# Kernel optimization log

Measured on AMD Instinct MI355X. Metric: run time of the kernel, lower is better.

## Reference

```python
import jax, jax.numpy as jnp
import numpy as np

B, N = 32, 512
NODE_F, EDGE_F = 64, 16
OUT = [64, 64, 64, 128]
TARGET = 16
DEGS = [1, 2, 3, 4]  # degree buckets (degree 0 filtered out, as in init_duvenaud)


def setup_inputs() -> dict:
    key = jax.random.key(0)
    ks = jax.random.split(key, 12)
    # adjacency: each node v connects to v+1..v+deg(v) (mod N), deg in {1..4}
    deg = jax.random.randint(ks[0], (B, N), 1, 5)
    off = jnp.arange(1, 5)                                   # (4,)
    cols = (jnp.arange(N)[:, None] + off[None, :]) % N       # (N,4)
    vals = (off[None, None, :] <= deg[:, :, None]).astype(jnp.float32)  # (B,N,4)
    g = jnp.zeros((B, N, N), jnp.float32).at[:, jnp.arange(N)[:, None], cols].set(vals)
    h_in = jax.random.normal(ks[1], (B, N, NODE_F), jnp.float32)
    e = jax.random.normal(ks[2], (B, N, N, EDGE_F), jnp.float32)
    # per-timestep, per-degree update matrices H_t: (n_deg, msg_in_t, out_t)
    ins = [NODE_F + EDGE_F, OUT[0] + EDGE_F, OUT[1] + EDGE_F]
    H0 = jax.random.normal(ks[3], (len(DEGS), ins[0], OUT[0]), jnp.float32)
    H1 = jax.random.normal(ks[4], (len(DEGS), ins[1], OUT[1]), jnp.float32)
    H2 = jax.random.normal(ks[5], (len(DEGS), ins[2], OUT[2]), jnp.float32)
    # readout matrices W_l for each of the 4 stored layers h^0..h^3
    layer_in = [NODE_F, OUT[0], OUT[1], OUT[2]]
    W0 = jax.random.normal(ks[6], (layer_in[0], OUT[3]), jnp.float32)
    W1 = jax.random.normal(ks[7], (layer_in[1], OUT[3]), jnp.float32)
    W2 = jax.random.normal(ks[8], (layer_in[2], OUT[3]), jnp.float32)
    W3 = jax.random.normal(ks[9], (layer_in[3], OUT[3]), jnp.float32)
    W_final = jax.random.normal(ks[10], (OUT[3], TARGET), jnp.float32) * 0.05
    b_final = jnp.zeros((TARGET,), jnp.float32)
    return {"g": g, "h_in": h_in, "e": e,
            "H0": H0, "H1": H1, "H2": H2,
            "W0": W0, "W1": W1, "W2": W2, "W3": W3,
            "W_final": W_final, "b_final": b_final}


def _step(g, e, h, H):
    # duvenaud message m_v = sum_w g[v,w] * cat(h_w, e_vw); split concat to avoid
    # materializing the (B,N,N,F+E) tensor the torch loop builds per node.
    mh = jnp.einsum('bvw,bwf->bvf', g, h)
    me = jnp.einsum('bvw,bvwe->bve', g, e)
    m = jnp.concatenate([mh, me], axis=-1)                 # (B,N,msg_in)
    deg = jnp.sum(g, axis=2)                               # (B,N) node degrees
    # degree-bucketed linear update: h'_v = m_v @ H[bucket(deg_v)]
    cand = jnp.einsum('bvm,dmo->bvdo', m, H)               # (B,N,n_deg,out)
    degs = jnp.asarray(DEGS, m.dtype)
    sel = (deg[:, :, None] == degs[None, None, :]).astype(m.dtype)  # one-hot bucket
    return jnp.einsum('bvd,bvdo->bvo', sel, cand)          # deg not in DEGS -> 0


def reference(g, h_in, e, H0, H1, H2, W0, W1, W2, W3, W_final, b_final):
    hs = [h_in]
    for H in (H0, H1, H2):
        hs.append(_step(g, e, hs[-1], H))
    # duvenaud readout: sum over layers/nodes of masked softmax(h_l @ W_l)
    acc = jnp.zeros((g.shape[0], W_final.shape[0]), h_in.dtype)
    for h, W in zip(hs, (W0, W1, W2, W3)):
        lin = jnp.einsum('bvf,fo->bvo', h, W)
        # mask rows whose linear output is all zero (padding / never-updated nodes)
        mask = (jnp.sum(lin != 0, axis=-1, keepdims=True) > 0).astype(lin.dtype)
        acc = acc + jnp.sum(jax.nn.softmax(lin, axis=-1) * mask, axis=1)
    out = acc @ W_final + b_final
    return jax.nn.softmax(out, axis=-1)
```

## Files before the change

### kernel.cpp

```cpp
#include <hip/hip_runtime.h>

#define BATCH 32
#define NN 512
#define NODE_F 64
#define EDGE_F 16
#define MSG 80
#define OUTF 64
#define RD 128
#define TGT 16
#define KMAX 8
#define ROWS (BATCH*NN)

__global__ __launch_bounds__(256) void preprocess_kernel(
    const float* __restrict__ g, const float* __restrict__ e,
    int* __restrict__ adj_idx, float* __restrict__ adj_val,
    int* __restrict__ nnzArr, int* __restrict__ bucketArr,
    float* __restrict__ me,
    float* __restrict__ h1, float* __restrict__ h2, float* __restrict__ h3,
    float* __restrict__ accv, int* __restrict__ counts)
{
  __shared__ int   s_idx[4][KMAX];
  __shared__ float s_val[4][KMAX];
  int tid  = threadIdx.x;
  int gtid = blockIdx.x * 256 + tid;
  if (gtid < BATCH*RD) accv[gtid] = 0.f;
  if (gtid < 4) counts[gtid] = 0;
  int lane = tid & 63;
  int wid  = tid >> 6;
  int row  = blockIdx.x * 4 + wid;
  const float* grow = g + (size_t)row * NN;
  float deg = 0.f;
  int cnt = 0;
  for (int it = 0; it < NN/64; ++it) {
    int w = it*64 + lane;
    float gv = grow[w];
    deg += gv;
    unsigned long long m = __ballot(gv != 0.0f);
    int before = __popcll(m & ((1ull << lane) - 1ull));
    if (gv != 0.0f) {
      int pos = cnt + before;
      if (pos < KMAX) { s_idx[wid][pos] = w; s_val[wid][pos] = gv; }
    }
    cnt += __popcll(m);
  }
  for (int off = 32; off; off >>= 1) deg += __shfl_xor(deg, off);
  __syncthreads();
  const float* erow = e + (size_t)row * NN * EDGE_F;
  if (cnt <= KMAX) {
    int k = lane >> 4, f = lane & 15;
    float part = 0.f;
    if (k < cnt)     part  = s_val[wid][k]   * erow[s_idx[wid][k]  *EDGE_F + f];
    if (cnt > 4) {
      int k2 = k + 4;
      if (k2 < cnt)  part += s_val[wid][k2]  * erow[s_idx[wid][k2] *EDGE_F + f];
    }
    part += __shfl_xor(part, 32);
    part += __shfl_xor(part, 16);
    if (lane < EDGE_F) me[(size_t)row*EDGE_F + lane] = part;
  } else {
    float mef = 0.f;
    for (int w = 0; w < NN; ++w) {
      float gv = grow[w];
      if (gv != 0.f && lane < EDGE_F) mef += gv * erow[w*EDGE_F + lane];
    }
    if (lane < EDGE_F) me[(size_t)row*EDGE_F + lane] = mef;
  }
  if (lane < KMAX && lane < cnt) {
    adj_idx[row*KMAX + lane] = s_idx[wid][lane];
    adj_val[row*KMAX + lane] = s_val[wid][lane];
  }
  int bk = -1;
  if      (deg == 1.0f) bk = 0;
  else if (deg == 2.0f) bk = 1;
  else if (deg == 3.0f) bk = 2;
  else if (deg == 4.0f) bk = 3;
  if (bk < 0) {
    h1[(size_t)row*NODE_F + lane] = 0.f;
    h2[(size_t)row*NODE_F + lane] = 0.f;
    h3[(size_t)row*NODE_F + lane] = 0.f;
  }
  if (lane == 0) {
    bucketArr[row] = bk;
    nnzArr[row] = cnt;
  }
}

__global__ __launch_bounds__(256) void scatter_kernel(
    const int* __restrict__ bucketArr,
    int* __restrict__ counts, int* __restrict__ perm)
{
  int i = blockIdx.x * blockDim.x + threadIdx.x;
  int lane = threadIdx.x & 63;
  int bk = bucketArr[i];
  #pragma unroll
  for (int d = 0; d < 4; ++d) {
    unsigned long long m = __ballot(bk == d);
    if (m == 0ull) continue;
    int leader = __ffsll((long long)m) - 1;
    int tot    = __popcll(m);
    int base = 0;
    if (lane == leader) base = atomicAdd(&counts[d], tot);
    base = __shfl(base, leader);
    if (bk == d) {
      int before = __popcll(m & ((1ull << lane) - 1ull));
      perm[d*ROWS + base + before] = i;
    }
  }
}

__global__ __launch_bounds__(256) void step_kernel(
    const float* __restrict__ h_prev, float* __restrict__ h_out,
    const float* __restrict__ Ht,
    const int* __restrict__ perm, const int* __restrict__ counts,
    const int* __restrict__ nnzArr, const int* __restrict__ adj_idx,
    const float* __restrict__ adj_val, const float* __restrict__ me,
    const float* __restrict__ g)
{
  int d = blockIdx.x >> 8;
  int chunk = blockIdx.x & 255;
  int cnt = counts[d];
  int base = chunk * 64;
  if (base >= cnt) return;
  __shared__ float smt[MSG][68];
  __shared__ float sH[MSG*OUTF];
  __shared__ int   srow[64];
  int tid = threadIdx.x;
  int lane = tid & 63, wid = tid >> 6;
  {
    const float4* H4 = (const float4*)(Ht + (size_t)d*MSG*OUTF);
    float4* s4 = (float4*)sH;
    for (int f = tid; f < MSG*OUTF/4; f += 256) s4[f] = H4[f];
  }
  #pragma unroll 2
  for (int t = 0; t < 16; ++t) {
    int nl = wid*16 + t;
    int gi = base + nl;
    float mh = 0.f;
    int row = -1;
    if (gi < cnt) {
      row = perm[d*ROWS + gi];
      int bb = row >> 9;
      int nnz = nnzArr[row];
      if (nnz <= KMAX) {
        int4   ai = *(const int4*)  &adj_idx[row*KMAX];
        float4 av = *(const float4*)&adj_val[row*KMAX];
        const float* hb = h_prev + (size_t)bb*NN*NODE_F + lane;
        if (nnz > 0) mh += av.x * hb[(size_t)ai.x*NODE_F];
        if (nnz > 1) mh += av.y * hb[(size_t)ai.y*NODE_F];
        if (nnz > 2) mh += av.z * hb[(size_t)ai.z*NODE_F];
        if (nnz > 3) mh += av.w * hb[(size_t)ai.w*NODE_F];
        if (nnz > 4) {
          int4   ai2 = *(const int4*)  &adj_idx[row*KMAX + 4];
          float4 av2 = *(const float4*)&adj_val[row*KMAX + 4];
          mh += av2.x * hb[(size_t)ai2.x*NODE_F];
          if (nnz > 5) mh += av2.y * hb[(size_t)ai2.y*NODE_F];
          if (nnz > 6) mh += av2.z * hb[(size_t)ai2.z*NODE_F];
          if (nnz > 7) mh += av2.w * hb[(size_t)ai2.w*NODE_F];
        }
      } else {
        const float* grow = g + (size_t)row * NN;
        for (int w = 0; w < NN; ++w) {
          float gv = grow[w];
          if (gv != 0.f) mh += gv * h_prev[((size_t)(bb*NN + w))*NODE_F + lane];
        }
      }
    }
    smt[lane][nl] = mh;
    if (lane < EDGE_F) smt[NODE_F + lane][nl] = (row >= 0) ? me[(size_t)row*EDGE_F + lane] : 0.f;
    if (lane == 0) srow[nl] = row;
  }
  __syncthreads();
  int tn = tid & 15, to = tid >> 4;
  float4 acc[4];
  acc[0] = acc[1] = acc[2] = acc[3] = make_float4(0.f,0.f,0.f,0.f);
  #pragma unroll 8
  for (int i = 0; i < MSG; ++i) {
    float4 hv = *(const float4*)&smt[i][4*tn];
    float4 wv = *(const float4*)&sH[i*OUTF + 4*to];
    float hk[4] = {hv.x, hv.y, hv.z, hv.w};
    #pragma unroll
    for (int k = 0; k < 4; ++k) {
      acc[k].x += hk[k]*wv.x; acc[k].y += hk[k]*wv.y;
      acc[k].z += hk[k]*wv.z; acc[k].w += hk[k]*wv.w;
    }
  }
  #pragma unroll
  for (int k = 0; k < 4; ++k) {
    int r = srow[4*tn + k];
    if (r >= 0) *(float4*)&h_out[(size_t)r*OUTF + 4*to] = acc[k];
  }
}

__global__ __launch_bounds__(256) void readout_kernel(
    const float* __restrict__ h0, const float* __restrict__ h1,
    const float* __restrict__ h2, const float* __restrict__ h3,
    const float* __restrict__ W0, const float* __restrict__ W1,
    const float* __restrict__ W2, const float* __restrict__ W3,
    float* __restrict__ accv)
{
  int l = blockIdx.x >> 8;
  int chunk = blockIdx.x & 255;
  const float* hs = (l==0)?h0:(l==1)?h1:(l==2)?h2:h3;
  const float* Wl = (l==0)?W0:(l==1)?W1:(l==2)?W2:W3;
  __shared__ float sW[NODE_F*RD];
  __shared__ float sht[NODE_F*68];
  __shared__ float snmax[64], snsum[64];
  __shared__ int   snflag[64];
  float* redm = sht;
  int*   redf = (int*)(sht + 64*17);
  int tid = threadIdx.x;
  {
    const float4* W4 = (const float4*)Wl;
    float4* sW4 = (float4*)sW;
    #pragma unroll
    for (int r = 0; r < 8; ++r) sW4[tid + 256*r] = W4[tid + 256*r];
    const float4* hv4 = (const float4*)(hs + (size_t)chunk*64*NODE_F);
    #pragma unroll
    for (int r = 0; r < 4; ++r) {
      int f = tid + 256*r;
      int n = f >> 4, c = f & 15;
      float4 v = hv4[f];
      sht[(4*c+0)*68 + n] = v.x;
      sht[(4*c+1)*68 + n] = v.y;
      sht[(4*c+2)*68 + n] = v.z;
      sht[(4*c+3)*68 + n] = v.w;
    }
  }
  __syncthreads();
  int tn = tid & 15, to = tid >> 4;
  int b = chunk >> 3;
  float4 accA[4], accB[4];
  #pragma unroll
  for (int k = 0; k < 4; ++k) { accA[k] = make_float4(0,0,0,0); accB[k] = make_float4(0,0,0,0); }
  #pragma unroll 4
  for (int i = 0; i < NODE_F; ++i) {
    float4 hv = *(const float4*)&sht[i*68 + 4*tn];
    float4 w0 = *(const float4*)&sW[i*128 + 8*to];
    float4 w1 = *(const float4*)&sW[i*128 + 8*to + 4];
    float hk[4] = {hv.x, hv.y, hv.z, hv.w};
    #pragma unroll
    for (int k = 0; k < 4; ++k) {
      accA[k].x += hk[k]*w0.x; accA[k].y += hk[k]*w0.y;
      accA[k].z += hk[k]*w0.z; accA[k].w += hk[k]*w0.w;
      accB[k].x += hk[k]*w1.x; accB[k].y += hk[k]*w1.y;
      accB[k].z += hk[k]*w1.z; accB[k].w += hk[k]*w1.w;
    }
  }
  __syncthreads();
  #pragma unroll
  for (int k = 0; k < 4; ++k) {
    float4 a = accA[k], bq = accB[k];
    float pm = fmaxf(fmaxf(fmaxf(a.x,a.y),fmaxf(a.z,a.w)),
                     fmaxf(fmaxf(bq.x,bq.y),fmaxf(bq.z,bq.w)));
    int nz = (a.x!=0.f)||(a.y!=0.f)||(a.z!=0.f)||(a.w!=0.f)||
             (bq.x!=0.f)||(bq.y!=0.f)||(bq.z!=0.f)||(bq.w!=0.f);
    int n = 4*tn + k;
    redm[n*17 + to] = pm;
    redf[n*17 + to] = nz;
  }
  __syncthreads();
  {
    int n = tid >> 2, sub = tid & 3;
    float m = redm[n*17 + sub*4 + 0];
    m = fmaxf(m, redm[n*17 + sub*4 + 1]);
    m = fmaxf(m, redm[n*17 + sub*4 + 2]);
    m = fmaxf(m, redm[n*17 + sub*4 + 3]);
    int f = redf[n*17 + sub*4 + 0] | redf[n*17 + sub*4 + 1] |
            redf[n*17 + sub*4 + 2] | redf[n*17 + sub*4 + 3];
    m = fmaxf(m, __shfl_xor(m, 1)); m = fmaxf(m, __shfl_xor(m, 2));
    f |= __shfl_xor(f, 1); f |= __shfl_xor(f, 2);
    if (sub == 0) { snmax[n] = m; snflag[n] = f; }
  }
  __syncthreads();
  #pragma unroll
  for (int k = 0; k < 4; ++k) {
    int n = 4*tn + k;
    float m = snmax[n];
    accA[k].x = __expf(accA[k].x - m); accA[k].y = __expf(accA[k].y - m);
    accA[k].z = __expf(accA[k].z - m); accA[k].w = __expf(accA[k].w - m);
    accB[k].x = __expf(accB[k].x - m); accB[k].y = __expf(accB[k].y - m);
    accB[k].z = __expf(accB[k].z - m); accB[k].w = __expf(accB[k].w - m);
    float ps = accA[k].x+accA[k].y+accA[k].z+accA[k].w+
               accB[k].x+accB[k].y+accB[k].z+accB[k].w;
    redm[n*17 + to] = ps;
  }
  __syncthreads();
  {
    int n = tid >> 2, sub = tid & 3;
    float s = redm[n*17 + sub*4 + 0] + redm[n*17 + sub*4 + 1] +
              redm[n*17 + sub*4 + 2] + redm[n*17 + sub*4 + 3];
    s += __shfl_xor(s, 1); s += __shfl_xor(s, 2);
    if (sub == 0) snsum[n] = s;
  }
  __syncthreads();
  float4 aj0 = make_float4(0,0,0,0), aj1 = make_float4(0,0,0,0);
  #pragma unroll
  for (int k = 0; k < 4; ++k) {
    int n = 4*tn + k;
    if (snflag[n]) {
      float inv = 1.0f / snsum[n];
      aj0.x += accA[k].x*inv; aj0.y += accA[k].y*inv;
      aj0.z += accA[k].z*inv; aj0.w += accA[k].w*inv;
      aj1.x += accB[k].x*inv; aj1.y += accB[k].y*inv;
      aj1.z += accB[k].z*inv; aj1.w += accB[k].w*inv;
    }
  }
  #pragma unroll
  for (int off = 1; off < 16; off <<= 1) {
    aj0.x += __shfl_xor(aj0.x, off); aj0.y += __shfl_xor(aj0.y, off);
    aj0.z += __shfl_xor(aj0.z, off); aj0.w += __shfl_xor(aj0.w, off);
    aj1.x += __shfl_xor(aj1.x, off); aj1.y += __shfl_xor(aj1.y, off);
    aj1.z += __shfl_xor(aj1.z, off); aj1.w += __shfl_xor(aj1.w, off);
  }
  if (tn == 0) {
    float* dst = &accv[b*RD + 8*to];
    atomicAdd(dst+0, aj0.x); atomicAdd(dst+1, aj0.y);
    atomicAdd(dst+2, aj0.z); atomicAdd(dst+3, aj0.w);
    atomicAdd(dst+4, aj1.x); atomicAdd(dst+5, aj1.y);
    atomicAdd(dst+6, aj1.z); atomicAdd(dst+7, aj1.w);
  }
}

__global__ __launch_bounds__(256) void final_kernel(
    const float* __restrict__ accv, const float* __restrict__ Wf,
    const float* __restrict__ bf, float* __restrict__ out)
{
  int b = blockIdx.x;
  int tid = threadIdx.x;
  int tg = tid & 15, part = tid >> 4;
  float p = 0.f;
  #pragma unroll
  for (int q = 0; q < 8; ++q) {
    int i = part*8 + q;
    p += accv[b*RD + i] * Wf[i*TGT + tg];
  }
  __shared__ float pp[16][17];
  pp[part][tg] = p;
  __syncthreads();
  if (tid < 16) {
    float v = bf[tid];
    #pragma unroll
    for (int q = 0; q < 16; ++q) v += pp[q][tid];
    float mx = v;
    for (int off = 8; off; off >>= 1) mx = fmaxf(mx, __shfl_xor(mx, off, 16));
    float e = __expf(v - mx);
    float s = e;
    for (int off = 8; off; off >>= 1) s += __shfl_xor(s, off, 16);
    out[b*TGT + tid] = e / s;
  }
}

extern "C" void kernel_launch(void* const* d_in, const int* in_sizes, int n_in,
                              void* d_out, int out_size, void* d_ws, size_t ws_size,
                              hipStream_t stream)
{
  const float* g    = (const float*)d_in[0];
  const float* h_in = (const float*)d_in[1];
  const float* e    = (const float*)d_in[2];
  const float* H0   = (const float*)d_in[3];
  const float* H1   = (const float*)d_in[4];
  const float* H2   = (const float*)d_in[5];
  const float* W0   = (const float*)d_in[6];
  const float* W1   = (const float*)d_in[7];
  const float* W2   = (const float*)d_in[8];
  const float* W3   = (const float*)d_in[9];
  const float* Wf   = (const float*)d_in[10];
  const float* bf   = (const float*)d_in[11];
  float* out = (float*)d_out;

  char* base = (char*)d_ws;
  size_t off = 0;
  auto alloc = [&](size_t bytes) -> void* {
    void* p = base + off;
    off = (off + bytes + 255) & ~(size_t)255;
    return p;
  };
  int*   adj_idx   = (int*)  alloc((size_t)ROWS*KMAX*sizeof(int));
  float* adj_val   = (float*)alloc((size_t)ROWS*KMAX*sizeof(float));
  int*   nnzArr    = (int*)  alloc((size_t)ROWS*sizeof(int));
  int*   bucketArr = (int*)  alloc((size_t)ROWS*sizeof(int));
  float* me        = (float*)alloc((size_t)ROWS*EDGE_F*sizeof(float));
  int*   perm      = (int*)  alloc((size_t)4*ROWS*sizeof(int));
  int*   counts    = (int*)  alloc(4*sizeof(int) + (size_t)BATCH*RD*sizeof(float));
  float* accv      = (float*)(counts + 4);
  float* h1        = (float*)alloc((size_t)ROWS*NODE_F*sizeof(float)*3);
  float* h2 = h1 + (size_t)ROWS*NODE_F;
  float* h3 = h2 + (size_t)ROWS*NODE_F;

  preprocess_kernel<<<ROWS/4, 256, 0, stream>>>(g, e, adj_idx, adj_val, nnzArr, bucketArr, me,
                                                h1, h2, h3, accv, counts);
  scatter_kernel<<<ROWS/256, 256, 0, stream>>>(bucketArr, counts, perm);
  step_kernel<<<4*256, 256, 0, stream>>>(h_in, h1, H0, perm, counts, nnzArr, adj_idx, adj_val, me, g);
  step_kernel<<<4*256, 256, 0, stream>>>(h1,   h2, H1, perm, counts, nnzArr, adj_idx, adj_val, me, g);
  step_kernel<<<4*256, 256, 0, stream>>>(h2,   h3, H2, perm, counts, nnzArr, adj_idx, adj_val, me, g);
  readout_kernel<<<4*256, 256, 0, stream>>>(h_in, h1, h2, h3, W0, W1, W2, W3, accv);
  final_kernel<<<BATCH, 256, 0, stream>>>(accv, Wf, bf, out);
}
```

Measured before the change: 770.5 us.

## Fuse layer-0 readout into scatter and final softmax into readout via last-block

Moves the layer-0 readout (which only needs h_in) into the scatter kernel as extra blocks, so it overlaps with the bucket scatter instead of running in the later readout. Merges the final projection and softmax into the readout kernel: the last block to finish, found with an atomic counter, does the final GEMV and softmax. This removes one kernel launch and shortens the tail of the readout, at the cost of a threadfence and atomic per block plus a serial single-block final stage.

```diff
diff --git a/kernel.cpp b/kernel.cpp
--- a/kernel.cpp
+++ b/kernel.cpp
@@ -10,6 +10,7 @@
 #define TGT 16
 #define KMAX 8
 #define ROWS (BATCH*NN)
+#define RB_TOTAL 768
 
 __global__ __launch_bounds__(256) void preprocess_kernel(
     const float* __restrict__ g, const float* __restrict__ e,
@@ -24,7 +25,7 @@
   int tid  = threadIdx.x;
   int gtid = blockIdx.x * 256 + tid;
   if (gtid < BATCH*RD) accv[gtid] = 0.f;
-  if (gtid < 4) counts[gtid] = 0;
+  if (gtid < 8) counts[gtid] = 0;
   int lane = tid & 63;
   int wid  = tid >> 6;
   int row  = blockIdx.x * 4 + wid;
@@ -85,26 +86,156 @@
   }
 }
 
-__global__ __launch_bounds__(256) void scatter_kernel(
+__device__ __forceinline__ void readout_block(
+    const float* __restrict__ hs, const float* __restrict__ Wl,
+    int chunk, float* __restrict__ accv,
+    float* sW, float* sht, float* snmax, float* snsum, int* snflag)
+{
+  float* redm = sht;
+  int*   redf = (int*)(sht + 64*17);
+  int tid = threadIdx.x;
+  {
+    const float4* W4 = (const float4*)Wl;
+    float4* sW4 = (float4*)sW;
+    #pragma unroll
+    for (int r = 0; r < 8; ++r) sW4[tid + 256*r] = W4[tid + 256*r];
+    const float4* hv4 = (const float4*)(hs + (size_t)chunk*64*NODE_F);
+    #pragma unroll
+    for (int r = 0; r < 4; ++r) {
+      int f = tid + 256*r;
+      int n = f >> 4, c = f & 15;
+      float4 v = hv4[f];
+      sht[(4*c+0)*68 + n] = v.x;
+      sht[(4*c+1)*68 + n] = v.y;
+      sht[(4*c+2)*68 + n] = v.z;
+      sht[(4*c+3)*68 + n] = v.w;
+    }
+  }
+  __syncthreads();
+  int tn = tid & 15, to = tid >> 4;
+  int b = chunk >> 3;
+  float4 accA[4], accB[4];
+  #pragma unroll
+  for (int k = 0; k < 4; ++k) { accA[k] = make_float4(0,0,0,0); accB[k] = make_float4(0,0,0,0); }
+  #pragma unroll 4
+  for (int i = 0; i < NODE_F; ++i) {
+    float4 hv = *(const float4*)&sht[i*68 + 4*tn];
+    float4 w0 = *(const float4*)&sW[i*128 + 8*to];
+    float4 w1 = *(const float4*)&sW[i*128 + 8*to + 4];
+    float hk[4] = {hv.x, hv.y, hv.z, hv.w};
+    #pragma unroll
+    for (int k = 0; k < 4; ++k) {
+      accA[k].x += hk[k]*w0.x; accA[k].y += hk[k]*w0.y;
+      accA[k].z += hk[k]*w0.z; accA[k].w += hk[k]*w0.w;
+      accB[k].x += hk[k]*w1.x; accB[k].y += hk[k]*w1.y;
+      accB[k].z += hk[k]*w1.z; accB[k].w += hk[k]*w1.w;
+    }
+  }
+  __syncthreads();
+  #pragma unroll
+  for (int k = 0; k < 4; ++k) {
+    float4 a = accA[k], bq = accB[k];
+    float pm = fmaxf(fmaxf(fmaxf(a.x,a.y),fmaxf(a.z,a.w)),
+                     fmaxf(fmaxf(bq.x,bq.y),fmaxf(bq.z,bq.w)));
+    int nz = (a.x!=0.f)||(a.y!=0.f)||(a.z!=0.f)||(a.w!=0.f)||
+             (bq.x!=0.f)||(bq.y!=0.f)||(bq.z!=0.f)||(bq.w!=0.f);
+    int n = 4*tn + k;
+    redm[n*17 + to] = pm;
+    redf[n*17 + to] = nz;
+  }
+  __syncthreads();
+  {
+    int n = tid >> 2, sub = tid & 3;
+    float m = redm[n*17 + sub*4 + 0];
+    m = fmaxf(m, redm[n*17 + sub*4 + 1]);
+    m = fmaxf(m, redm[n*17 + sub*4 + 2]);
+    m = fmaxf(m, redm[n*17 + sub*4 + 3]);
+    int f = redf[n*17 + sub*4 + 0] | redf[n*17 + sub*4 + 1] |
+            redf[n*17 + sub*4 + 2] | redf[n*17 + sub*4 + 3];
+    m = fmaxf(m, __shfl_xor(m, 1)); m = fmaxf(m, __shfl_xor(m, 2));
+    f |= __shfl_xor(f, 1); f |= __shfl_xor(f, 2);
+    if (sub == 0) { snmax[n] = m; snflag[n] = f; }
+  }
+  __syncthreads();
+  #pragma unroll
+  for (int k = 0; k < 4; ++k) {
+    int n = 4*tn + k;
+    float m = snmax[n];
+    accA[k].x = __expf(accA[k].x - m); accA[k].y = __expf(accA[k].y - m);
+    accA[k].z = __expf(accA[k].z - m); accA[k].w = __expf(accA[k].w - m);
+    accB[k].x = __expf(accB[k].x - m); accB[k].y = __expf(accB[k].y - m);
+    accB[k].z = __expf(accB[k].z - m); accB[k].w = __expf(accB[k].w - m);
+    float ps = accA[k].x+accA[k].y+accA[k].z+accA[k].w+
+               accB[k].x+accB[k].y+accB[k].z+accB[k].w;
+    redm[n*17 + to] = ps;
+  }
+  __syncthreads();
+  {
+    int n = tid >> 2, sub = tid & 3;
+    float s = redm[n*17 + sub*4 + 0] + redm[n*17 + sub*4 + 1] +
+              redm[n*17 + sub*4 + 2] + redm[n*17 + sub*4 + 3];
+    s += __shfl_xor(s, 1); s += __shfl_xor(s, 2);
+    if (sub == 0) snsum[n] = s;
+  }
+  __syncthreads();
+  float4 aj0 = make_float4(0,0,0,0), aj1 = make_float4(0,0,0,0);
+  #pragma unroll
+  for (int k = 0; k < 4; ++k) {
+    int n = 4*tn + k;
+    if (snflag[n]) {
+      float inv = 1.0f / snsum[n];
+      aj0.x += accA[k].x*inv; aj0.y += accA[k].y*inv;
+      aj0.z += accA[k].z*inv; aj0.w += accA[k].w*inv;
+      aj1.x += accB[k].x*inv; aj1.y += accB[k].y*inv;
+      aj1.z += accB[k].z*inv; aj1.w += accB[k].w*inv;
+    }
+  }
+  #pragma unroll
+  for (int off = 1; off < 16; off <<= 1) {
+    aj0.x += __shfl_xor(aj0.x, off); aj0.y += __shfl_xor(aj0.y, off);
+    aj0.z += __shfl_xor(aj0.z, off); aj0.w += __shfl_xor(aj0.w, off);
+    aj1.x += __shfl_xor(aj1.x, off); aj1.y += __shfl_xor(aj1.y, off);
+    aj1.z += __shfl_xor(aj1.z, off); aj1.w += __shfl_xor(aj1.w, off);
+  }
+  if (tn == 0) {
+    float* dst = &accv[b*RD + 8*to];
+    atomicAdd(dst+0, aj0.x); atomicAdd(dst+1, aj0.y);
+    atomicAdd(dst+2, aj0.z); atomicAdd(dst+3, aj0.w);
+    atomicAdd(dst+4, aj1.x); atomicAdd(dst+5, aj1.y);
+    atomicAdd(dst+6, aj1.z); atomicAdd(dst+7, aj1.w);
+  }
+}
+
+__global__ __launch_bounds__(256) void scatter_l0_kernel(
     const int* __restrict__ bucketArr,
-    int* __restrict__ counts, int* __restrict__ perm)
-{
-  int i = blockIdx.x * blockDim.x + threadIdx.x;
-  int lane = threadIdx.x & 63;
-  int bk = bucketArr[i];
-  #pragma unroll
-  for (int d = 0; d < 4; ++d) {
-    unsigned long long m = __ballot(bk == d);
-    if (m == 0ull) continue;
-    int leader = __ffsll((long long)m) - 1;
-    int tot    = __popcll(m);
-    int base = 0;
-    if (lane == leader) base = atomicAdd(&counts[d], tot);
-    base = __shfl(base, leader);
-    if (bk == d) {
-      int before = __popcll(m & ((1ull << lane) - 1ull));
-      perm[d*ROWS + base + before] = i;
-    }
+    int* __restrict__ counts, int* __restrict__ perm,
+    const float* __restrict__ h_in, const float* __restrict__ W0,
+    float* __restrict__ accv)
+{
+  __shared__ float sW[NODE_F*RD];
+  __shared__ float sht[NODE_F*68];
+  __shared__ float snmax[64], snsum[64];
+  __shared__ int   snflag[64];
+  if (blockIdx.x < 64) {
+    int i = blockIdx.x * blockDim.x + threadIdx.x;
+    int lane = threadIdx.x & 63;
+    int bk = bucketArr[i];
+    #pragma unroll
+    for (int d = 0; d < 4; ++d) {
+      unsigned long long m = __ballot(bk == d);
+      if (m == 0ull) continue;
+      int leader = __ffsll((long long)m) - 1;
+      int tot    = __popcll(m);
+      int base = 0;
+      if (lane == leader) base = atomicAdd(&counts[d], tot);
+      base = __shfl(base, leader);
+      if (bk == d) {
+        int before = __popcll(m & ((1ull << lane) - 1ull));
+        perm[d*ROWS + base + before] = i;
+      }
+    }
+  } else {
+    readout_block(h_in, W0, blockIdx.x - 64, accv, sW, sht, snmax, snsum, snflag);
   }
 }
 
@@ -191,162 +322,53 @@
   }
 }
 
-__global__ __launch_bounds__(256) void readout_kernel(
-    const float* __restrict__ h0, const float* __restrict__ h1,
-    const float* __restrict__ h2, const float* __restrict__ h3,
-    const float* __restrict__ W0, const float* __restrict__ W1,
-    const float* __restrict__ W2, const float* __restrict__ W3,
-    float* __restrict__ accv)
-{
-  int l = blockIdx.x >> 8;
-  int chunk = blockIdx.x & 255;
-  const float* hs = (l==0)?h0:(l==1)?h1:(l==2)?h2:h3;
-  const float* Wl = (l==0)?W0:(l==1)?W1:(l==2)?W2:W3;
+__global__ __launch_bounds__(256) void readout_final_kernel(
+    const float* __restrict__ h1, const float* __restrict__ h2,
+    const float* __restrict__ h3,
+    const float* __restrict__ W1, const float* __restrict__ W2,
+    const float* __restrict__ W3,
+    float* __restrict__ accv, int* __restrict__ done,
+    const float* __restrict__ Wf, const float* __restrict__ bf,
+    float* __restrict__ out)
+{
   __shared__ float sW[NODE_F*RD];
   __shared__ float sht[NODE_F*68];
   __shared__ float snmax[64], snsum[64];
   __shared__ int   snflag[64];
-  float* redm = sht;
-  int*   redf = (int*)(sht + 64*17);
+  __shared__ int   s_last;
+  int l = blockIdx.x >> 8;
+  int chunk = blockIdx.x & 255;
+  const float* hs = (l==0)?h1:(l==1)?h2:h3;
+  const float* Wl = (l==0)?W1:(l==1)?W2:W3;
+  readout_block(hs, Wl, chunk, accv, sW, sht, snmax, snsum, snflag);
   int tid = threadIdx.x;
-  {
-    const float4* W4 = (const float4*)Wl;
-    float4* sW4 = (float4*)sW;
-    #pragma unroll
-    for (int r = 0; r < 8; ++r) sW4[tid + 256*r] = W4[tid + 256*r];
-    const float4* hv4 = (const float4*)(hs + (size_t)chunk*64*NODE_F);
-    #pragma unroll
-    for (int r = 0; r < 4; ++r) {
-      int f = tid + 256*r;
-      int n = f >> 4, c = f & 15;
-      float4 v = hv4[f];
-      sht[(4*c+0)*68 + n] = v.x;
-      sht[(4*c+1)*68 + n] = v.y;
-      sht[(4*c+2)*68 + n] = v.z;
-      sht[(4*c+3)*68 + n] = v.w;
-    }
-  }
-  __syncthreads();
-  int tn = tid & 15, to = tid >> 4;
-  int b = chunk >> 3;
-  float4 accA[4], accB[4];
-  #pragma unroll
-  for (int k = 0; k < 4; ++k) { accA[k] = make_float4(0,0,0,0); accB[k] = make_float4(0,0,0,0); }
-  #pragma unroll 4
-  for (int i = 0; i < NODE_F; ++i) {
-    float4 hv = *(const float4*)&sht[i*68 + 4*tn];
-    float4 w0 = *(const float4*)&sW[i*128 + 8*to];
-    float4 w1 = *(const float4*)&sW[i*128 + 8*to + 4];
-    float hk[4] = {hv.x, hv.y, hv.z, hv.w};
-    #pragma unroll
-    for (int k = 0; k < 4; ++k) {
-      accA[k].x += hk[k]*w0.x; accA[k].y += hk[k]*w0.y;
-      accA[k].z += hk[k]*w0.z; accA[k].w += hk[k]*w0.w;
-      accB[k].x += hk[k]*w1.x; accB[k].y += hk[k]*w1.y;
-      accB[k].z += hk[k]*w1.z; accB[k].w += hk[k]*w1.w;
-    }
-  }
-  __syncthreads();
-  #pragma unroll
-  for (int k = 0; k < 4; ++k) {
-    float4 a = accA[k], bq = accB[k];
-    float pm = fmaxf(fmaxf(fmaxf(a.x,a.y),fmaxf(a.z,a.w)),
-                     fmaxf(fmaxf(bq.x,bq.y),fmaxf(bq.z,bq.w)));
-    int nz = (a.x!=0.f)||(a.y!=0.f)||(a.z!=0.f)||(a.w!=0.f)||
-             (bq.x!=0.f)||(bq.y!=0.f)||(bq.z!=0.f)||(bq.w!=0.f);
-    int n = 4*tn + k;
-    redm[n*17 + to] = pm;
-    redf[n*17 + to] = nz;
-  }
-  __syncthreads();
-  {
-    int n = tid >> 2, sub = tid & 3;
-    float m = redm[n*17 + sub*4 + 0];
-    m = fmaxf(m, redm[n*17 + sub*4 + 1]);
-    m = fmaxf(m, redm[n*17 + sub*4 + 2]);
-    m = fmaxf(m, redm[n*17 + sub*4 + 3]);
-    int f = redf[n*17 + sub*4 + 0] | redf[n*17 + sub*4 + 1] |
-            redf[n*17 + sub*4 + 2] | redf[n*17 + sub*4 + 3];
-    m = fmaxf(m, __shfl_xor(m, 1)); m = fmaxf(m, __shfl_xor(m, 2));
-    f |= __shfl_xor(f, 1); f |= __shfl_xor(f, 2);
-    if (sub == 0) { snmax[n] = m; snflag[n] = f; }
-  }
-  __syncthreads();
-  #pragma unroll
-  for (int k = 0; k < 4; ++k) {
-    int n = 4*tn + k;
-    float m = snmax[n];
-    accA[k].x = __expf(accA[k].x - m); accA[k].y = __expf(accA[k].y - m);
-    accA[k].z = __expf(accA[k].z - m); accA[k].w = __expf(accA[k].w - m);
-    accB[k].x = __expf(accB[k].x - m); accB[k].y = __expf(accB[k].y - m);
-    accB[k].z = __expf(accB[k].z - m); accB[k].w = __expf(accB[k].w - m);
-    float ps = accA[k].x+accA[k].y+accA[k].z+accA[k].w+
-               accB[k].x+accB[k].y+accB[k].z+accB[k].w;
-    redm[n*17 + to] = ps;
-  }
-  __syncthreads();
-  {
-    int n = tid >> 2, sub = tid & 3;
-    float s = redm[n*17 + sub*4 + 0] + redm[n*17 + sub*4 + 1] +
-              redm[n*17 + sub*4 + 2] + redm[n*17 + sub*4 + 3];
-    s += __shfl_xor(s, 1); s += __shfl_xor(s, 2);
-    if (sub == 0) snsum[n] = s;
-  }
-  __syncthreads();
-  float4 aj0 = make_float4(0,0,0,0), aj1 = make_float4(0,0,0,0);
-  #pragma unroll
-  for (int k = 0; k < 4; ++k) {
-    int n = 4*tn + k;
-    if (snflag[n]) {
-      float inv = 1.0f / snsum[n];
-      aj0.x += accA[k].x*inv; aj0.y += accA[k].y*inv;
-      aj0.z += accA[k].z*inv; aj0.w += accA[k].w*inv;
-      aj1.x += accB[k].x*inv; aj1.y += accB[k].y*inv;
-      aj1.z += accB[k].z*inv; aj1.w += accB[k].w*inv;
-    }
-  }
-  #pragma unroll
-  for (int off = 1; off < 16; off <<= 1) {
-    aj0.x += __shfl_xor(aj0.x, off); aj0.y += __shfl_xor(aj0.y, off);
-    aj0.z += __shfl_xor(aj0.z, off); aj0.w += __shfl_xor(aj0.w, off);
-    aj1.x += __shfl_xor(aj1.x, off); aj1.y += __shfl_xor(aj1.y, off);
-    aj1.z += __shfl_xor(aj1.z, off); aj1.w += __shfl_xor(aj1.w, off);
-  }
-  if (tn == 0) {
-    float* dst = &accv[b*RD + 8*to];
-    atomicAdd(dst+0, aj0.x); atomicAdd(dst+1, aj0.y);
-    atomicAdd(dst+2, aj0.z); atomicAdd(dst+3, aj0.w);
-    atomicAdd(dst+4, aj1.x); atomicAdd(dst+5, aj1.y);
-    atomicAdd(dst+6, aj1.z); atomicAdd(dst+7, aj1.w);
-  }
-}
-
-__global__ __launch_bounds__(256) void final_kernel(
-    const float* __restrict__ accv, const float* __restrict__ Wf,
-    const float* __restrict__ bf, float* __restrict__ out)
-{
-  int b = blockIdx.x;
-  int tid = threadIdx.x;
-  int tg = tid & 15, part = tid >> 4;
-  float p = 0.f;
-  #pragma unroll
-  for (int q = 0; q < 8; ++q) {
-    int i = part*8 + q;
-    p += accv[b*RD + i] * Wf[i*TGT + tg];
-  }
-  __shared__ float pp[16][17];
-  pp[part][tg] = p;
-  __syncthreads();
-  if (tid < 16) {
-    float v = bf[tid];
-    #pragma unroll
-    for (int q = 0; q < 16; ++q) v += pp[q][tid];
-    float mx = v;
-    for (int off = 8; off; off >>= 1) mx = fmaxf(mx, __shfl_xor(mx, off, 16));
-    float e = __expf(v - mx);
-    float s = e;
-    for (int off = 8; off; off >>= 1) s += __shfl_xor(s, off, 16);
-    out[b*TGT + tid] = e / s;
+  __threadfence();
+  __syncthreads();
+  if (tid == 0) s_last = (atomicAdd(done, 1) == RB_TOTAL - 1) ? 1 : 0;
+  __syncthreads();
+  if (s_last) {
+    __threadfence();
+    float* sacc = sW;
+    #pragma unroll
+    for (int r = 0; r < 16; ++r) {
+      int j = r*256 + tid;
+      sacc[j] = __hip_atomic_load(&accv[j], __ATOMIC_RELAXED, __HIP_MEMORY_SCOPE_AGENT);
+    }
+    __syncthreads();
+    #pragma unroll
+    for (int rep = 0; rep < 2; ++rep) {
+      int idx = rep*256 + tid;
+      int b = idx >> 4, tg = idx & 15;
+      float v = bf[tg];
+      #pragma unroll 8
+      for (int i = 0; i < RD; ++i) v += sacc[b*RD + i] * Wf[i*TGT + tg];
+      float mx = v;
+      for (int off = 8; off; off >>= 1) mx = fmaxf(mx, __shfl_xor(mx, off, 16));
+      float e2 = __expf(v - mx);
+      float s = e2;
+      for (int off = 8; off; off >>= 1) s += __shfl_xor(s, off, 16);
+      out[b*TGT + tg] = e2 / s;
+    }
   }
 }
 
@@ -381,18 +403,19 @@
   int*   bucketArr = (int*)  alloc((size_t)ROWS*sizeof(int));
   float* me        = (float*)alloc((size_t)ROWS*EDGE_F*sizeof(float));
   int*   perm      = (int*)  alloc((size_t)4*ROWS*sizeof(int));
-  int*   counts    = (int*)  alloc(4*sizeof(int) + (size_t)BATCH*RD*sizeof(float));
-  float* accv      = (float*)(counts + 4);
+  int*   counts    = (int*)  alloc(8*sizeof(int) + (size_t)BATCH*RD*sizeof(float));
+  int*   done      = counts + 4;
+  float* accv      = (float*)(counts + 8);
   float* h1        = (float*)alloc((size_t)ROWS*NODE_F*sizeof(float)*3);
   float* h2 = h1 + (size_t)ROWS*NODE_F;
   float* h3 = h2 + (size_t)ROWS*NODE_F;
 
   preprocess_kernel<<<ROWS/4, 256, 0, stream>>>(g, e, adj_idx, adj_val, nnzArr, bucketArr, me,
                                                 h1, h2, h3, accv, counts);
-  scatter_kernel<<<ROWS/256, 256, 0, stream>>>(bucketArr, counts, perm);
+  scatter_l0_kernel<<<64 + 256, 256, 0, stream>>>(bucketArr, counts, perm, h_in, W0, accv);
   step_kernel<<<4*256, 256, 0, stream>>>(h_in, h1, H0, perm, counts, nnzArr, adj_idx, adj_val, me, g);
   step_kernel<<<4*256, 256, 0, stream>>>(h1,   h2, H1, perm, counts, nnzArr, adj_idx, adj_val, me, g);
   step_kernel<<<4*256, 256, 0, stream>>>(h2,   h3, H2, perm, counts, nnzArr, adj_idx, adj_val, me, g);
-  readout_kernel<<<4*256, 256, 0, stream>>>(h_in, h1, h2, h3, W0, W1, W2, W3, accv);
-  final_kernel<<<BATCH, 256, 0, stream>>>(accv, Wf, bf, out);
-}
+  readout_final_kernel<<<RB_TOTAL, 256, 0, stream>>>(h1, h2, h3, W1, W2, W3,
+                                                     accv, done, Wf, bf, out);
+}
```

After: 809.7 us. 5.1% more time.

## Fuse per-layer readout blocks into step kernels to overlap with message passing

Applied to the files above, without the earlier changes.

The readout for layer l is computed by extra blocks appended to the step kernel that produces layer l+1, since h_l is already available. Only the layer-3 readout stays in a separate small kernel. This removes the standalone 1024-block readout launch and lets readout work fill idle CUs while step blocks run, at the cost of a shared-memory union and a larger grid per step. Total time is probably dominated by preprocessing the dense g and e tensors, so the effect is likely small.

```diff
diff --git a/kernel.cpp b/kernel.cpp
--- a/kernel.cpp
+++ b/kernel.cpp
@@ -10,6 +10,8 @@
 #define TGT 16
 #define KMAX 8
 #define ROWS (BATCH*NN)
+#define STEP_BLKS 1024
+#define RO_BLKS 256
 
 __global__ __launch_bounds__(256) void preprocess_kernel(
     const float* __restrict__ g, const float* __restrict__ e,
@@ -24,7 +26,7 @@
   int tid  = threadIdx.x;
   int gtid = blockIdx.x * 256 + tid;
   if (gtid < BATCH*RD) accv[gtid] = 0.f;
-  if (gtid < 4) counts[gtid] = 0;
+  if (gtid < 8) counts[gtid] = 0;
   int lane = tid & 63;
   int wid  = tid >> 6;
   int row  = blockIdx.x * 4 + wid;
@@ -108,27 +110,158 @@
   }
 }
 
-__global__ __launch_bounds__(256) void step_kernel(
+union StepRO {
+  struct { float smt[MSG][68]; float sH[MSG*OUTF]; int srow[64]; } s;
+  struct { float sW[NODE_F*RD]; float sht[NODE_F*68];
+           float snmax[64]; float snsum[64]; int snflag[64]; } r;
+};
+
+__device__ __forceinline__ void readout_block(
+    const float* __restrict__ hs, const float* __restrict__ Wl,
+    int chunk, float* __restrict__ accv,
+    float* sW, float* sht, float* snmax, float* snsum, int* snflag)
+{
+  float* redm = sht;
+  int*   redf = (int*)(sht + 64*17);
+  int tid = threadIdx.x;
+  {
+    const float4* W4 = (const float4*)Wl;
+    float4* sW4 = (float4*)sW;
+    #pragma unroll
+    for (int r = 0; r < 8; ++r) sW4[tid + 256*r] = W4[tid + 256*r];
+    const float4* hv4 = (const float4*)(hs + (size_t)chunk*64*NODE_F);
+    #pragma unroll
+    for (int r = 0; r < 4; ++r) {
+      int f = tid + 256*r;
+      int n = f >> 4, c = f & 15;
+      float4 v = hv4[f];
+      sht[(4*c+0)*68 + n] = v.x;
+      sht[(4*c+1)*68 + n] = v.y;
+      sht[(4*c+2)*68 + n] = v.z;
+      sht[(4*c+3)*68 + n] = v.w;
+    }
+  }
+  __syncthreads();
+  int tn = tid & 15, to = tid >> 4;
+  int b = chunk >> 3;
+  float4 accA[4], accB[4];
+  #pragma unroll
+  for (int k = 0; k < 4; ++k) { accA[k] = make_float4(0,0,0,0); accB[k] = make_float4(0,0,0,0); }
+  #pragma unroll 4
+  for (int i = 0; i < NODE_F; ++i) {
+    float4 hv = *(const float4*)&sht[i*68 + 4*tn];
+    float4 w0 = *(const float4*)&sW[i*128 + 8*to];
+    float4 w1 = *(const float4*)&sW[i*128 + 8*to + 4];
+    float hk[4] = {hv.x, hv.y, hv.z, hv.w};
+    #pragma unroll
+    for (int k = 0; k < 4; ++k) {
+      accA[k].x += hk[k]*w0.x; accA[k].y += hk[k]*w0.y;
+      accA[k].z += hk[k]*w0.z; accA[k].w += hk[k]*w0.w;
+      accB[k].x += hk[k]*w1.x; accB[k].y += hk[k]*w1.y;
+      accB[k].z += hk[k]*w1.z; accB[k].w += hk[k]*w1.w;
+    }
+  }
+  __syncthreads();
+  #pragma unroll
+  for (int k = 0; k < 4; ++k) {
+    float4 a = accA[k], bq = accB[k];
+    float pm = fmaxf(fmaxf(fmaxf(a.x,a.y),fmaxf(a.z,a.w)),
+                     fmaxf(fmaxf(bq.x,bq.y),fmaxf(bq.z,bq.w)));
+    int nz = (a.x!=0.f)||(a.y!=0.f)||(a.z!=0.f)||(a.w!=0.f)||
+             (bq.x!=0.f)||(bq.y!=0.f)||(bq.z!=0.f)||(bq.w!=0.f);
+    int n = 4*tn + k;
+    redm[n*17 + to] = pm;
+    redf[n*17 + to] = nz;
+  }
+  __syncthreads();
+  {
+    int n = tid >> 2, sub = tid & 3;
+    float m = redm[n*17 + sub*4 + 0];
+    m = fmaxf(m, redm[n*17 + sub*4 + 1]);
+    m = fmaxf(m, redm[n*17 + sub*4 + 2]);
+    m = fmaxf(m, redm[n*17 + sub*4 + 3]);
+    int f = redf[n*17 + sub*4 + 0] | redf[n*17 + sub*4 + 1] |
+            redf[n*17 + sub*4 + 2] | redf[n*17 + sub*4 + 3];
+    m = fmaxf(m, __shfl_xor(m, 1)); m = fmaxf(m, __shfl_xor(m, 2));
+    f |= __shfl_xor(f, 1); f |= __shfl_xor(f, 2);
+    if (sub == 0) { snmax[n] = m; snflag[n] = f; }
+  }
+  __syncthreads();
+  #pragma unroll
+  for (int k = 0; k < 4; ++k) {
+    int n = 4*tn + k;
+    float m = snmax[n];
+    accA[k].x = __expf(accA[k].x - m); accA[k].y = __expf(accA[k].y - m);
+    accA[k].z = __expf(accA[k].z - m); accA[k].w = __expf(accA[k].w - m);
+    accB[k].x = __expf(accB[k].x - m); accB[k].y = __expf(accB[k].y - m);
+    accB[k].z = __expf(accB[k].z - m); accB[k].w = __expf(accB[k].w - m);
+    float ps = accA[k].x+accA[k].y+accA[k].z+accA[k].w+
+               accB[k].x+accB[k].y+accB[k].z+accB[k].w;
+    redm[n*17 + to] = ps;
+  }
+  __syncthreads();
+  {
+    int n = tid >> 2, sub = tid & 3;
+    float s = redm[n*17 + sub*4 + 0] + redm[n*17 + sub*4 + 1] +
+              redm[n*17 + sub*4 + 2] + redm[n*17 + sub*4 + 3];
+    s += __shfl_xor(s, 1); s += __shfl_xor(s, 2);
+    if (sub == 0) snsum[n] = s;
+  }
+  __syncthreads();
+  float4 aj0 = make_float4(0,0,0,0), aj1 = make_float4(0,0,0,0);
+  #pragma unroll
+  for (int k = 0; k < 4; ++k) {
+    int n = 4*tn + k;
+    if (snflag[n]) {
+      float inv = 1.0f / snsum[n];
+      aj0.x += accA[k].x*inv; aj0.y += accA[k].y*inv;
+      aj0.z += accA[k].z*inv; aj0.w += accA[k].w*inv;
+      aj1.x += accB[k].x*inv; aj1.y += accB[k].y*inv;
+      aj1.z += accB[k].z*inv; aj1.w += accB[k].w*inv;
+    }
+  }
+  #pragma unroll
+  for (int off = 1; off < 16; off <<= 1) {
+    aj0.x += __shfl_xor(aj0.x, off); aj0.y += __shfl_xor(aj0.y, off);
+    aj0.z += __shfl_xor(aj0.z, off); aj0.w += __shfl_xor(aj0.w, off);
+    aj1.x += __shfl_xor(aj1.x, off); aj1.y += __shfl_xor(aj1.y, off);
+    aj1.z += __shfl_xor(aj1.z, off); aj1.w += __shfl_xor(aj1.w, off);
+  }
+  if (tn == 0) {
+    float* dst = &accv[b*RD + 8*to];
+    atomicAdd(dst+0, aj0.x); atomicAdd(dst+1, aj0.y);
+    atomicAdd(dst+2, aj0.z); atomicAdd(dst+3, aj0.w);
+    atomicAdd(dst+4, aj1.x); atomicAdd(dst+5, aj1.y);
+    atomicAdd(dst+6, aj1.z); atomicAdd(dst+7, aj1.w);
+  }
+}
+
+__global__ __launch_bounds__(256) void step_ro_kernel(
     const float* __restrict__ h_prev, float* __restrict__ h_out,
     const float* __restrict__ Ht,
     const int* __restrict__ perm, const int* __restrict__ counts,
     const int* __restrict__ nnzArr, const int* __restrict__ adj_idx,
     const float* __restrict__ adj_val, const float* __restrict__ me,
-    const float* __restrict__ g)
-{
+    const float* __restrict__ g,
+    const float* __restrict__ h_ro, const float* __restrict__ W_ro,
+    float* __restrict__ accv)
+{
+  __shared__ StepRO u;
+  int tid = threadIdx.x;
+  if (blockIdx.x >= STEP_BLKS) {
+    readout_block(h_ro, W_ro, blockIdx.x - STEP_BLKS, accv,
+                  u.r.sW, u.r.sht, u.r.snmax, u.r.snsum, u.r.snflag);
+    return;
+  }
   int d = blockIdx.x >> 8;
   int chunk = blockIdx.x & 255;
   int cnt = counts[d];
   int base = chunk * 64;
   if (base >= cnt) return;
-  __shared__ float smt[MSG][68];
-  __shared__ float sH[MSG*OUTF];
-  __shared__ int   srow[64];
-  int tid = threadIdx.x;
   int lane = tid & 63, wid = tid >> 6;
   {
     const float4* H4 = (const float4*)(Ht + (size_t)d*MSG*OUTF);
-    float4* s4 = (float4*)sH;
+    float4* s4 = (float4*)u.s.sH;
     for (int f = tid; f < MSG*OUTF/4; f += 256) s4[f] = H4[f];
   }
   #pragma unroll 2
@@ -165,9 +298,9 @@
         }
       }
     }
-    smt[lane][nl] = mh;
-    if (lane < EDGE_F) smt[NODE_F + lane][nl] = (row >= 0) ? me[(size_t)row*EDGE_F + lane] : 0.f;
-    if (lane == 0) srow[nl] = row;
+    u.s.smt[lane][nl] = mh;
+    if (lane < EDGE_F) u.s.smt[NODE_F + lane][nl] = (row >= 0) ? me[(size_t)row*EDGE_F + lane] : 0.f;
+    if (lane == 0) u.s.srow[nl] = row;
   }
   __syncthreads();
   int tn = tid & 15, to = tid >> 4;
@@ -175,8 +308,8 @@
   acc[0] = acc[1] = acc[2] = acc[3] = make_float4(0.f,0.f,0.f,0.f);
   #pragma unroll 8
   for (int i = 0; i < MSG; ++i) {
-    float4 hv = *(const float4*)&smt[i][4*tn];
-    float4 wv = *(const float4*)&sH[i*OUTF + 4*to];
+    float4 hv = *(const float4*)&u.s.smt[i][4*tn];
+    float4 wv = *(const float4*)&u.s.sH[i*OUTF + 4*to];
     float hk[4] = {hv.x, hv.y, hv.z, hv.w};
     #pragma unroll
     for (int k = 0; k < 4; ++k) {
@@ -186,139 +319,18 @@
   }
   #pragma unroll
   for (int k = 0; k < 4; ++k) {
-    int r = srow[4*tn + k];
+    int r = u.s.srow[4*tn + k];
     if (r >= 0) *(float4*)&h_out[(size_t)r*OUTF + 4*to] = acc[k];
   }
 }
 
-__global__ __launch_bounds__(256) void readout_kernel(
-    const float* __restrict__ h0, const float* __restrict__ h1,
-    const float* __restrict__ h2, const float* __restrict__ h3,
-    const float* __restrict__ W0, const float* __restrict__ W1,
-    const float* __restrict__ W2, const float* __restrict__ W3,
+__global__ __launch_bounds__(256) void readout_l3_kernel(
+    const float* __restrict__ h3, const float* __restrict__ W3,
     float* __restrict__ accv)
 {
-  int l = blockIdx.x >> 8;
-  int chunk = blockIdx.x & 255;
-  const float* hs = (l==0)?h0:(l==1)?h1:(l==2)?h2:h3;
-  const float* Wl = (l==0)?W0:(l==1)?W1:(l==2)?W2:W3;
-  __shared__ float sW[NODE_F*RD];
-  __shared__ float sht[NODE_F*68];
-  __shared__ float snmax[64], snsum[64];
-  __shared__ int   snflag[64];
-  float* redm = sht;
-  int*   redf = (int*)(sht + 64*17);
-  int tid = threadIdx.x;
-  {
-    const float4* W4 = (const float4*)Wl;
-    float4* sW4 = (float4*)sW;
-    #pragma unroll
-    for (int r = 0; r < 8; ++r) sW4[tid + 256*r] = W4[tid + 256*r];
-    const float4* hv4 = (const float4*)(hs + (size_t)chunk*64*NODE_F);
-    #pragma unroll
-    for (int r = 0; r < 4; ++r) {
-      int f = tid + 256*r;
-      int n = f >> 4, c = f & 15;
-      float4 v = hv4[f];
-      sht[(4*c+0)*68 + n] = v.x;
-      sht[(4*c+1)*68 + n] = v.y;
-      sht[(4*c+2)*68 + n] = v.z;
-      sht[(4*c+3)*68 + n] = v.w;
-    }
-  }
-  __syncthreads();
-  int tn = tid & 15, to = tid >> 4;
-  int b = chunk >> 3;
-  float4 accA[4], accB[4];
-  #pragma unroll
-  for (int k = 0; k < 4; ++k) { accA[k] = make_float4(0,0,0,0); accB[k] = make_float4(0,0,0,0); }
-  #pragma unroll 4
-  for (int i = 0; i < NODE_F; ++i) {
-    float4 hv = *(const float4*)&sht[i*68 + 4*tn];
-    float4 w0 = *(const float4*)&sW[i*128 + 8*to];
-    float4 w1 = *(const float4*)&sW[i*128 + 8*to + 4];
-    float hk[4] = {hv.x, hv.y, hv.z, hv.w};
-    #pragma unroll
-    for (int k = 0; k < 4; ++k) {
-      accA[k].x += hk[k]*w0.x; accA[k].y += hk[k]*w0.y;
-      accA[k].z += hk[k]*w0.z; accA[k].w += hk[k]*w0.w;
-      accB[k].x += hk[k]*w1.x; accB[k].y += hk[k]*w1.y;
-      accB[k].z += hk[k]*w1.z; accB[k].w += hk[k]*w1.w;
-    }
-  }
-  __syncthreads();
-  #pragma unroll
-  for (int k = 0; k < 4; ++k) {
-    float4 a = accA[k], bq = accB[k];
-    float pm = fmaxf(fmaxf(fmaxf(a.x,a.y),fmaxf(a.z,a.w)),
-                     fmaxf(fmaxf(bq.x,bq.y),fmaxf(bq.z,bq.w)));
-    int nz = (a.x!=0.f)||(a.y!=0.f)||(a.z!=0.f)||(a.w!=0.f)||
-             (bq.x!=0.f)||(bq.y!=0.f)||(bq.z!=0.f)||(bq.w!=0.f);
-    int n = 4*tn + k;
-    redm[n*17 + to] = pm;
-    redf[n*17 + to] = nz;
-  }
-  __syncthreads();
-  {
-    int n = tid >> 2, sub = tid & 3;
-    float m = redm[n*17 + sub*4 + 0];
-    m = fmaxf(m, redm[n*17 + sub*4 + 1]);
-    m = fmaxf(m, redm[n*17 + sub*4 + 2]);
-    m = fmaxf(m, redm[n*17 + sub*4 + 3]);
-    int f = redf[n*17 + sub*4 + 0] | redf[n*17 + sub*4 + 1] |
-            redf[n*17 + sub*4 + 2] | redf[n*17 + sub*4 + 3];
-    m = fmaxf(m, __shfl_xor(m, 1)); m = fmaxf(m, __shfl_xor(m, 2));
-    f |= __shfl_xor(f, 1); f |= __shfl_xor(f, 2);
-    if (sub == 0) { snmax[n] = m; snflag[n] = f; }
-  }
-  __syncthreads();
-  #pragma unroll
-  for (int k = 0; k < 4; ++k) {
-    int n = 4*tn + k;
-    float m = snmax[n];
-    accA[k].x = __expf(accA[k].x - m); accA[k].y = __expf(accA[k].y - m);
-    accA[k].z = __expf(accA[k].z - m); accA[k].w = __expf(accA[k].w - m);
-    accB[k].x = __expf(accB[k].x - m); accB[k].y = __expf(accB[k].y - m);
-    accB[k].z = __expf(accB[k].z - m); accB[k].w = __expf(accB[k].w - m);
-    float ps = accA[k].x+accA[k].y+accA[k].z+accA[k].w+
-               accB[k].x+accB[k].y+accB[k].z+accB[k].w;
-    redm[n*17 + to] = ps;
-  }
-  __syncthreads();
-  {
-    int n = tid >> 2, sub = tid & 3;
-    float s = redm[n*17 + sub*4 + 0] + redm[n*17 + sub*4 + 1] +
-              redm[n*17 + sub*4 + 2] + redm[n*17 + sub*4 + 3];
-    s += __shfl_xor(s, 1); s += __shfl_xor(s, 2);
-    if (sub == 0) snsum[n] = s;
-  }
-  __syncthreads();
-  float4 aj0 = make_float4(0,0,0,0), aj1 = make_float4(0,0,0,0);
-  #pragma unroll
-  for (int k = 0; k < 4; ++k) {
-    int n = 4*tn + k;
-    if (snflag[n]) {
-      float inv = 1.0f / snsum[n];
-      aj0.x += accA[k].x*inv; aj0.y += accA[k].y*inv;
-      aj0.z += accA[k].z*inv; aj0.w += accA[k].w*inv;
-      aj1.x += accB[k].x*inv; aj1.y += accB[k].y*inv;
-      aj1.z += accB[k].z*inv; aj1.w += accB[k].w*inv;
-    }
-  }
-  #pragma unroll
-  for (int off = 1; off < 16; off <<= 1) {
-    aj0.x += __shfl_xor(aj0.x, off); aj0.y += __shfl_xor(aj0.y, off);
-    aj0.z += __shfl_xor(aj0.z, off); aj0.w += __shfl_xor(aj0.w, off);
-    aj1.x += __shfl_xor(aj1.x, off); aj1.y += __shfl_xor(aj1.y, off);
-    aj1.z += __shfl_xor(aj1.z, off); aj1.w += __shfl_xor(aj1.w, off);
-  }
-  if (tn == 0) {
-    float* dst = &accv[b*RD + 8*to];
-    atomicAdd(dst+0, aj0.x); atomicAdd(dst+1, aj0.y);
-    atomicAdd(dst+2, aj0.z); atomicAdd(dst+3, aj0.w);
-    atomicAdd(dst+4, aj1.x); atomicAdd(dst+5, aj1.y);
-    atomicAdd(dst+6, aj1.z); atomicAdd(dst+7, aj1.w);
-  }
+  __shared__ StepRO u;
+  readout_block(h3, W3, blockIdx.x, accv,
+                u.r.sW, u.r.sht, u.r.snmax, u.r.snsum, u.r.snflag);
 }
 
 __global__ __launch_bounds__(256) void final_kernel(
@@ -381,8 +393,8 @@
   int*   bucketArr = (int*)  alloc((size_t)ROWS*sizeof(int));
   float* me        = (float*)alloc((size_t)ROWS*EDGE_F*sizeof(float));
   int*   perm      = (int*)  alloc((size_t)4*ROWS*sizeof(int));
-  int*   counts    = (int*)  alloc(4*sizeof(int) + (size_t)BATCH*RD*sizeof(float));
-  float* accv      = (float*)(counts + 4);
+  int*   counts    = (int*)  alloc(8*sizeof(int) + (size_t)BATCH*RD*sizeof(float));
+  float* accv      = (float*)(counts + 8);
   float* h1        = (float*)alloc((size_t)ROWS*NODE_F*sizeof(float)*3);
   float* h2 = h1 + (size_t)ROWS*NODE_F;
   float* h3 = h2 + (size_t)ROWS*NODE_F;
@@ -390,9 +402,12 @@
   preprocess_kernel<<<ROWS/4, 256, 0, stream>>>(g, e, adj_idx, adj_val, nnzArr, bucketArr, me,
                                                 h1, h2, h3, accv, counts);
   scatter_kernel<<<ROWS/256, 256, 0, stream>>>(bucketArr, counts, perm);
-  step_kernel<<<4*256, 256, 0, stream>>>(h_in, h1, H0, perm, counts, nnzArr, adj_idx, adj_val, me, g);
-  step_kernel<<<4*256, 256, 0, stream>>>(h1,   h2, H1, perm, counts, nnzArr, adj_idx, adj_val, me, g);
-  step_kernel<<<4*256, 256, 0, stream>>>(h2,   h3, H2, perm, counts, nnzArr, adj_idx, adj_val, me, g);
-  readout_kernel<<<4*256, 256, 0, stream>>>(h_in, h1, h2, h3, W0, W1, W2, W3, accv);
+  step_ro_kernel<<<STEP_BLKS + RO_BLKS, 256, 0, stream>>>(
+      h_in, h1, H0, perm, counts, nnzArr, adj_idx, adj_val, me, g, h_in, W0, accv);
+  step_ro_kernel<<<STEP_BLKS + RO_BLKS, 256, 0, stream>>>(
+      h1,   h2, H1, perm, counts, nnzArr, adj_idx, adj_val, me, g, h1,   W1, accv);
+  step_ro_kernel<<<STEP_BLKS + RO_BLKS, 256, 0, stream>>>(
+      h2,   h3, H2, perm, counts, nnzArr, adj_idx, adj_val, me, g, h2,   W2, accv);
+  readout_l3_kernel<<<RO_BLKS, 256, 0, stream>>>(h3, W3, accv);
   final_kernel<<<BATCH, 256, 0, stream>>>(accv, Wf, bf, out);
 }
```

After: 759.0 us. No clear change (-1.5%).
